# Performance work log

Hardware: AMD Instinct MI355X
Metric: run time of the kernel (lower is better)

Reference implementation:

```python
import jax, jax.numpy as jnp
import numpy as np

N = 100000   # nodes
E = 3200000  # edges (avg degree 32)
G = 1024     # graphs in batch
H = 16       # hidden_dim


def setup_inputs() -> dict:
    key = jax.random.key(0)
    ks = jax.random.split(key, 12)
    p = lambda k, s: jax.random.normal(k, s, dtype=jnp.float32) * 0.1
    return {
        "types": jax.random.randint(ks[0], (N,), 0, 3),
        "pos": jax.random.randint(ks[1], (N,), 0, 3),
        "edge_index": jax.random.randint(ks[2], (2, E), 0, N),
        "batch": jnp.sort(jax.random.randint(ks[3], (N,), 0, G)),
        "W1": p(ks[4], (3, H)), "b1": jnp.zeros((H,), jnp.float32),
        "W2": p(ks[5], (3, H)), "b2": jnp.zeros((H,), jnp.float32),
        "Wg0": p(ks[6], (2 * H, H)), "bg0": jnp.zeros((H,), jnp.float32),
        "Wg1": p(ks[7], (H, H)), "bg1": jnp.zeros((H,), jnp.float32),
        "Wg2": p(ks[8], (H, H)), "bg2": jnp.zeros((H,), jnp.float32),
        "Wo": p(ks[9], (H, 1)), "bo": jnp.zeros((1,), jnp.float32),
    }


def reference(types, pos, edge_index, batch, W1, b1, W2, b2,
              Wg0, bg0, Wg1, bg1, Wg2, bg2, Wo, bo):
    # one-hot encode + linear embed
    xt = jax.nn.one_hot(types, 3, dtype=jnp.float32) @ W1 + b1   # [N, H]
    xp = jax.nn.one_hot(pos, 3, dtype=jnp.float32) @ W2 + b2     # [N, H]
    z = jnp.concatenate([xt, xp], axis=-1)                        # [N, 2H]

    src, dst = edge_index[0], edge_index[1]
    # GCN symmetric normalization with self-loops (gcn_norm)
    deg = jax.ops.segment_sum(jnp.ones((E,), jnp.float32), dst, num_segments=N) + 1.0
    dis = jax.lax.rsqrt(deg)                                      # D^{-1/2}
    edge_coef = (dis[src] * dis[dst])[:, None]                    # [E, 1]
    self_coef = (dis * dis)[:, None]                              # [N, 1]

    def gcn_conv(x, W, b):
        h = x @ W                                                 # [N, H]
        agg = jax.ops.segment_sum(h[src] * edge_coef, dst, num_segments=N)
        return agg + h * self_coef + b

    z = jax.nn.relu(gcn_conv(z, Wg0, bg0))  # dropout=0.2 is train-only; eval mode
    z = jax.nn.relu(gcn_conv(z, Wg1, bg1))
    z = gcn_conv(z, Wg2, bg2)               # no act after last layer

    # global_mean_pool over graph ids
    cnt = jax.ops.segment_sum(jnp.ones((N,), jnp.float32), batch, num_segments=G)
    pooled = jax.ops.segment_sum(z, batch, num_segments=G) / jnp.maximum(cnt, 1.0)[:, None]
    return pooled @ Wo + bo                                       # [G, 1]
```

## Files before the change

kernel.cpp:

```cpp
#include <hip/hip_runtime.h>
#include <hip/hip_fp16.h>

#define NN 100000
#define NE 3200000
#define NG 1024
#define NP 100352
#define NBUCK 391
#define NBLK 256
#define CHUNK ((NE + NBLK - 1) / NBLK)
#define WINCAP 12288

static __device__ inline void acc_u2(float4& acc, uint2 u) {
    __half2* ph = reinterpret_cast<__half2*>(&u);
    float2 lo = __half22float2(ph[0]);
    float2 hi = __half22float2(ph[1]);
    acc.x += lo.x; acc.y += lo.y; acc.z += hi.x; acc.w += hi.y;
}
static __device__ inline uint2 pack4(float a, float b, float c, float d) {
    __half2 lo = __floats2half2_rn(a, b);
    __half2 hi = __floats2half2_rn(c, d);
    uint2 u;
    u.x = *reinterpret_cast<unsigned int*>(&lo);
    u.y = *reinterpret_cast<unsigned int*>(&hi);
    return u;
}
static __device__ inline float4 shfl_xor4(float4 v, int m) {
    float4 r;
    r.x = __shfl_xor(v.x, m); r.y = __shfl_xor(v.y, m);
    r.z = __shfl_xor(v.z, m); r.w = __shfl_xor(v.w, m);
    return r;
}

__global__ void hist_buckets(const int* __restrict__ dst, int* __restrict__ bcnt) {
    __shared__ int sm[NBUCK];
    int tid = threadIdx.x;
    for (int i = tid; i < NBUCK; i += 256) sm[i] = 0;
    __syncthreads();
    int s = blockIdx.x * CHUNK, e = min(NE, s + CHUNK);
    for (int i = s + tid; i < e; i += 256) atomicAdd(&sm[dst[i] >> 8], 1);
    __syncthreads();
    for (int i = tid; i < NBUCK; i += 256)
        if (sm[i]) atomicAdd(&bcnt[i], sm[i]);
}

__global__ void scan_buckets(const int* __restrict__ bcnt, int* __restrict__ bbase) {
    __shared__ int tmp[512];
    int tid = threadIdx.x;
    int v = (tid < NBUCK) ? bcnt[tid] : 0;
    tmp[tid] = v;
    __syncthreads();
    for (int off = 1; off < 512; off <<= 1) {
        int t = (tid >= off) ? tmp[tid - off] : 0;
        __syncthreads();
        tmp[tid] += t;
        __syncthreads();
    }
    if (tid < NBUCK) bbase[tid] = tmp[tid] - v;
}

__global__ void partition(const int* __restrict__ src, const int* __restrict__ dst,
                          const int* __restrict__ bbase, int* __restrict__ bfill,
                          int* __restrict__ part) {
    __shared__ int smh[NBUCK];
    __shared__ int smc[NBUCK];
    int tid = threadIdx.x;
    for (int i = tid; i < NBUCK; i += 256) smh[i] = 0;
    __syncthreads();
    int s = blockIdx.x * CHUNK, e = min(NE, s + CHUNK);
    for (int i = s + tid; i < e; i += 256) atomicAdd(&smh[dst[i] >> 8], 1);
    __syncthreads();
    for (int i = tid; i < NBUCK; i += 256) {
        int c = smh[i];
        smc[i] = c ? (bbase[i] + atomicAdd(&bfill[i], c)) : 0;
    }
    __syncthreads();
    for (int i = s + tid; i < e; i += 256) {
        int d = dst[i];
        int b = d >> 8;
        int p = atomicAdd(&smc[b], 1);
        part[p] = src[i] | ((d & 255) << 17);
    }
}

__global__ void build_csr(const int* __restrict__ part, const int* __restrict__ bbase,
                          const int* __restrict__ bcnt, int* __restrict__ cnt,
                          int* __restrict__ offs, float* __restrict__ dis,
                          int* __restrict__ srcs) {
    __shared__ int sm_cnt[256];
    __shared__ int sm_off[256];
    __shared__ int sm_cur[256];
    __shared__ int sm_win[WINCAP];
    int b = blockIdx.x, tid = threadIdx.x;
    int base = bbase[b], m = bcnt[b];
    sm_cnt[tid] = 0;
    __syncthreads();
    for (int i = tid; i < m; i += 256) atomicAdd(&sm_cnt[part[base + i] >> 17], 1);
    __syncthreads();
    int v = sm_cnt[tid];
    sm_off[tid] = v;
    __syncthreads();
    for (int off = 1; off < 256; off <<= 1) {
        int t = (tid >= off) ? sm_off[tid - off] : 0;
        __syncthreads();
        sm_off[tid] += t;
        __syncthreads();
    }
    int excl = sm_off[tid] - v;
    int n = b * 256 + tid;
    if (n < NN) {
        cnt[n] = v;
        offs[n] = base + excl;
        dis[n] = rsqrtf((float)v + 1.0f);
    }
    sm_cur[tid] = excl;
    __syncthreads();
    if (m <= WINCAP) {
        for (int i = tid; i < m; i += 256) {
            int p = part[base + i];
            int l = atomicAdd(&sm_cur[p >> 17], 1);
            sm_win[l] = p & 0x1FFFF;
        }
        __syncthreads();
        for (int i = tid; i < m; i += 256) srcs[base + i] = sm_win[i];
    } else {
        for (int i = tid; i < m; i += 256) {
            int p = part[base + i];
            int l = atomicAdd(&sm_cur[p >> 17], 1);
            srcs[base + l] = p & 0x1FFFF;
        }
    }
}

__global__ void embed_tf0(const int* __restrict__ types, const int* __restrict__ pos,
                          const float* __restrict__ W1, const float* __restrict__ b1,
                          const float* __restrict__ W2, const float* __restrict__ b2,
                          const float* __restrict__ Wg0, const float* __restrict__ dis,
                          uint2* __restrict__ hs) {
    __shared__ float sW[32 * 16];
    int tid = threadIdx.x;
    sW[tid] = Wg0[tid];
    sW[tid + 256] = Wg0[tid + 256];
    __syncthreads();
    int n = blockIdx.x * 256 + tid;
    if (n >= NN) return;
    int ty = types[n], pp = pos[n];
    float z[32];
#pragma unroll
    for (int j = 0; j < 16; j++) z[j] = W1[ty * 16 + j] + b1[j];
#pragma unroll
    for (int j = 0; j < 16; j++) z[16 + j] = W2[pp * 16 + j] + b2[j];
    float dn = dis[n];
    uint2 o[4];
#pragma unroll
    for (int q = 0; q < 4; q++) {
        float hv[4];
#pragma unroll
        for (int m = 0; m < 4; m++) {
            float a = 0.0f;
#pragma unroll
            for (int k = 0; k < 32; k++) a += z[k] * sW[k * 16 + q * 4 + m];
            hv[m] = a * dn;
        }
        o[q] = pack4(hv[0], hv[1], hv[2], hv[3]);
    }
#pragma unroll
    for (int q = 0; q < 4; q++) hs[(size_t)n * 4 + q] = o[q];
}

template <int RELU, int FUSE_POOL>
__global__ void agg_tf(const uint2* __restrict__ hs, const int* __restrict__ srcs,
                       const int* __restrict__ offs, const int* __restrict__ cnt,
                       const float* __restrict__ dis, const float* __restrict__ bias,
                       const float* __restrict__ Wn, uint2* __restrict__ hs_out,
                       const int* __restrict__ batch,
                       float* __restrict__ pool, int* __restrict__ gcnt) {
    __shared__ float sW[256];
    int tid = threadIdx.x;
    if (!FUSE_POOL) {
        sW[tid] = Wn[tid];
        __syncthreads();
    }
    int gid = blockIdx.x * 256 + tid;
    int n = gid >> 2, q = gid & 3;
    if (n >= NN) return;
    int beg = offs[n], deg = cnt[n];
    float dn = dis[n];
    float4 acc = make_float4(0.f, 0.f, 0.f, 0.f);
    int i = 0;
    for (; i + 4 <= deg; i += 4) {
        int s0 = srcs[beg + i + 0];
        int s1 = srcs[beg + i + 1];
        int s2 = srcs[beg + i + 2];
        int s3 = srcs[beg + i + 3];
        uint2 a0 = hs[(size_t)s0 * 4 + q];
        uint2 a1 = hs[(size_t)s1 * 4 + q];
        uint2 a2 = hs[(size_t)s2 * 4 + q];
        uint2 a3 = hs[(size_t)s3 * 4 + q];
        acc_u2(acc, a0); acc_u2(acc, a1); acc_u2(acc, a2); acc_u2(acc, a3);
    }
    for (; i < deg; i++) {
        int s = srcs[beg + i];
        acc_u2(acc, hs[(size_t)s * 4 + q]);
    }
    acc_u2(acc, hs[(size_t)n * 4 + q]);
    float4 b4 = ((const float4*)bias)[q];
    acc.x = fmaf(acc.x, dn, b4.x);
    acc.y = fmaf(acc.y, dn, b4.y);
    acc.z = fmaf(acc.z, dn, b4.z);
    acc.w = fmaf(acc.w, dn, b4.w);
    if (RELU) {
        acc.x = fmaxf(acc.x, 0.f); acc.y = fmaxf(acc.y, 0.f);
        acc.z = fmaxf(acc.z, 0.f); acc.w = fmaxf(acc.w, 0.f);
    }
    if (FUSE_POOL) {
        float4 w4 = ((const float4*)Wn)[q];
        float s = acc.x * w4.x + acc.y * w4.y + acc.z * w4.z + acc.w * w4.w;
        s += __shfl_xor(s, 1);
        s += __shfl_xor(s, 2);
        if (q == 0) {
            int g = batch[n];
            atomicAdd(&pool[g], s);
            atomicAdd(&gcnt[g], 1);
        }
    } else {
        float4 vals[4];
        vals[0] = acc;
        vals[1] = shfl_xor4(acc, 1);
        vals[2] = shfl_xor4(acc, 2);
        vals[3] = shfl_xor4(acc, 3);
        const float4* sW4 = (const float4*)sW;
        float4 hv = make_float4(0.f, 0.f, 0.f, 0.f);
#pragma unroll
        for (int m = 0; m < 4; m++) {
            float4 v = vals[m];
            int rb = (q ^ m) << 2;
            float4 w;
            w = sW4[(rb + 0) * 4 + q];
            hv.x += v.x * w.x; hv.y += v.x * w.y; hv.z += v.x * w.z; hv.w += v.x * w.w;
            w = sW4[(rb + 1) * 4 + q];
            hv.x += v.y * w.x; hv.y += v.y * w.y; hv.z += v.y * w.z; hv.w += v.y * w.w;
            w = sW4[(rb + 2) * 4 + q];
            hv.x += v.z * w.x; hv.y += v.z * w.y; hv.z += v.z * w.z; hv.w += v.z * w.w;
            w = sW4[(rb + 3) * 4 + q];
            hv.x += v.w * w.x; hv.y += v.w * w.y; hv.z += v.w * w.z; hv.w += v.w * w.w;
        }
        hs_out[(size_t)n * 4 + q] = pack4(hv.x * dn, hv.y * dn, hv.z * dn, hv.w * dn);
    }
}

__global__ void finalize(const float* __restrict__ pool, const int* __restrict__ gcnt,
                         const float* __restrict__ bo, float* __restrict__ out) {
    int g = blockIdx.x * 256 + threadIdx.x;
    if (g < NG) {
        float c = fmaxf((float)gcnt[g], 1.0f);
        out[g] = pool[g] / c + bo[0];
    }
}

extern "C" void kernel_launch(void* const* d_in, const int* in_sizes, int n_in,
                              void* d_out, int out_size, void* d_ws, size_t ws_size,
                              hipStream_t stream) {
    const int*   types = (const int*)d_in[0];
    const int*   pos   = (const int*)d_in[1];
    const int*   ei    = (const int*)d_in[2];
    const int*   batch = (const int*)d_in[3];
    const float* W1  = (const float*)d_in[4];
    const float* b1  = (const float*)d_in[5];
    const float* W2  = (const float*)d_in[6];
    const float* b2  = (const float*)d_in[7];
    const float* Wg0 = (const float*)d_in[8];
    const float* bg0 = (const float*)d_in[9];
    const float* Wg1 = (const float*)d_in[10];
    const float* bg1 = (const float*)d_in[11];
    const float* Wg2 = (const float*)d_in[12];
    const float* bg2 = (const float*)d_in[13];
    const float* Wo  = (const float*)d_in[14];
    const float* bo  = (const float*)d_in[15];
    float* out = (float*)d_out;

    const int* esrc = ei;
    const int* edst = ei + NE;

    int*   bcnt  = (int*)d_ws;
    int*   bfill = bcnt + 512;
    float* pool  = (float*)(bfill + 512);
    int*   gcnt  = (int*)(pool + NG);
    int*   bbase = gcnt + NG;
    int*   cnt   = bbase + 512;
    int*   offs  = cnt + NP;
    float* dis   = (float*)(offs + NP);
    int*   srcs  = (int*)(dis + NP);
    int*   part  = srcs + NE;
    uint2* hsA   = (uint2*)part;
    uint2* hsB   = (uint2*)(part + NE / 2);
    (void)ws_size; (void)n_in; (void)in_sizes; (void)out_size;

    hipMemsetAsync(d_ws, 0, (size_t)(1024 + 2 * NG) * sizeof(int), stream);

    const int NB256 = (NN + 255) / 256;
    const int QB = (NN * 4 + 255) / 256;

    hist_buckets<<<NBLK, 256, 0, stream>>>(edst, bcnt);
    scan_buckets<<<1, 512, 0, stream>>>(bcnt, bbase);
    partition<<<NBLK, 256, 0, stream>>>(esrc, edst, bbase, bfill, part);
    build_csr<<<NBUCK, 256, 0, stream>>>(part, bbase, bcnt, cnt, offs, dis, srcs);

    embed_tf0<<<NB256, 256, 0, stream>>>(types, pos, W1, b1, W2, b2, Wg0, dis, hsA);
    agg_tf<1, 0><<<QB, 256, 0, stream>>>(hsA, srcs, offs, cnt, dis, bg0, Wg1, hsB,
                                         batch, pool, gcnt);
    agg_tf<1, 0><<<QB, 256, 0, stream>>>(hsB, srcs, offs, cnt, dis, bg1, Wg2, hsA,
                                         batch, pool, gcnt);
    agg_tf<0, 1><<<QB, 256, 0, stream>>>(hsA, srcs, offs, cnt, dis, bg2, Wo, hsB ,
                                         batch, pool, gcnt);

    finalize<<<(NG + 255) / 256, 256, 0, stream>>>(pool, gcnt, bo, out);
}
```

Measured before the change: 333.5 us.

## Replace CSR gather with bucketed edge-parallel LDS-atomic aggregation

Drops the per-node CSR build (scan and reorder into srcs) and aggregates directly from the bucket-partitioned edge list. Each block, split four ways per 256-node bucket, accumulates 16-wide rows into shared memory with atomics, then flushes to a global fp32 buffer with global atomics. A separate per-node kernel applies bias, ReLU and the next weight matrix. This removes the CSR construction pass and the per-node degree imbalance, at the cost of heavy LDS atomic traffic, extra global atomics, a 6.4MB fp32 intermediate that is read and rezeroed each layer, and more kernel launches.

```diff
diff --git a/kernel.cpp b/kernel.cpp
--- a/kernel.cpp
+++ b/kernel.cpp
@@ -8,14 +8,8 @@
 #define NBUCK 391
 #define NBLK 256
 #define CHUNK ((NE + NBLK - 1) / NBLK)
-#define WINCAP 12288
-
-static __device__ inline void acc_u2(float4& acc, uint2 u) {
-    __half2* ph = reinterpret_cast<__half2*>(&u);
-    float2 lo = __half22float2(ph[0]);
-    float2 hi = __half22float2(ph[1]);
-    acc.x += lo.x; acc.y += lo.y; acc.z += hi.x; acc.w += hi.y;
-}
+#define SPLIT_LOG2 2
+
 static __device__ inline uint2 pack4(float a, float b, float c, float d) {
     __half2 lo = __floats2half2_rn(a, b);
     __half2 hi = __floats2half2_rn(c, d);
@@ -24,12 +18,6 @@
     u.y = *reinterpret_cast<unsigned int*>(&hi);
     return u;
 }
-static __device__ inline float4 shfl_xor4(float4 v, int m) {
-    float4 r;
-    r.x = __shfl_xor(v.x, m); r.y = __shfl_xor(v.y, m);
-    r.z = __shfl_xor(v.z, m); r.w = __shfl_xor(v.w, m);
-    return r;
-}
 
 __global__ void hist_buckets(const int* __restrict__ dst, int* __restrict__ bcnt) {
     __shared__ int sm[NBUCK];
@@ -82,53 +70,17 @@
     }
 }
 
-__global__ void build_csr(const int* __restrict__ part, const int* __restrict__ bbase,
-                          const int* __restrict__ bcnt, int* __restrict__ cnt,
-                          int* __restrict__ offs, float* __restrict__ dis,
-                          int* __restrict__ srcs) {
-    __shared__ int sm_cnt[256];
-    __shared__ int sm_off[256];
-    __shared__ int sm_cur[256];
-    __shared__ int sm_win[WINCAP];
+__global__ void deg_dis(const int* __restrict__ part, const int* __restrict__ bbase,
+                        const int* __restrict__ bcnt, float* __restrict__ dis) {
+    __shared__ int smc[256];
     int b = blockIdx.x, tid = threadIdx.x;
+    smc[tid] = 0;
+    __syncthreads();
     int base = bbase[b], m = bcnt[b];
-    sm_cnt[tid] = 0;
-    __syncthreads();
-    for (int i = tid; i < m; i += 256) atomicAdd(&sm_cnt[part[base + i] >> 17], 1);
-    __syncthreads();
-    int v = sm_cnt[tid];
-    sm_off[tid] = v;
-    __syncthreads();
-    for (int off = 1; off < 256; off <<= 1) {
-        int t = (tid >= off) ? sm_off[tid - off] : 0;
-        __syncthreads();
-        sm_off[tid] += t;
-        __syncthreads();
-    }
-    int excl = sm_off[tid] - v;
+    for (int i = base + tid; i < base + m; i += 256) atomicAdd(&smc[part[i] >> 17], 1);
+    __syncthreads();
     int n = b * 256 + tid;
-    if (n < NN) {
-        cnt[n] = v;
-        offs[n] = base + excl;
-        dis[n] = rsqrtf((float)v + 1.0f);
-    }
-    sm_cur[tid] = excl;
-    __syncthreads();
-    if (m <= WINCAP) {
-        for (int i = tid; i < m; i += 256) {
-            int p = part[base + i];
-            int l = atomicAdd(&sm_cur[p >> 17], 1);
-            sm_win[l] = p & 0x1FFFF;
-        }
-        __syncthreads();
-        for (int i = tid; i < m; i += 256) srcs[base + i] = sm_win[i];
-    } else {
-        for (int i = tid; i < m; i += 256) {
-            int p = part[base + i];
-            int l = atomicAdd(&sm_cur[p >> 17], 1);
-            srcs[base + l] = p & 0x1FFFF;
-        }
-    }
+    if (n < NN) dis[n] = rsqrtf((float)smc[tid] + 1.0f);
 }
 
 __global__ void embed_tf0(const int* __restrict__ types, const int* __restrict__ pos,
@@ -167,84 +119,135 @@
     for (int q = 0; q < 4; q++) hs[(size_t)n * 4 + q] = o[q];
 }
 
+static __device__ inline void acc16(float* __restrict__ ap, uint4 a, uint4 b) {
+    const __half2* h = reinterpret_cast<const __half2*>(&a);
+    const __half2* g = reinterpret_cast<const __half2*>(&b);
+    float2 f0 = __half22float2(h[0]), f1 = __half22float2(h[1]);
+    float2 f2 = __half22float2(h[2]), f3 = __half22float2(h[3]);
+    float2 f4 = __half22float2(g[0]), f5 = __half22float2(g[1]);
+    float2 f6 = __half22float2(g[2]), f7 = __half22float2(g[3]);
+    atomicAdd(ap + 0, f0.x);  atomicAdd(ap + 1, f0.y);
+    atomicAdd(ap + 2, f1.x);  atomicAdd(ap + 3, f1.y);
+    atomicAdd(ap + 4, f2.x);  atomicAdd(ap + 5, f2.y);
+    atomicAdd(ap + 6, f3.x);  atomicAdd(ap + 7, f3.y);
+    atomicAdd(ap + 8, f4.x);  atomicAdd(ap + 9, f4.y);
+    atomicAdd(ap + 10, f5.x); atomicAdd(ap + 11, f5.y);
+    atomicAdd(ap + 12, f6.x); atomicAdd(ap + 13, f6.y);
+    atomicAdd(ap + 14, f7.x); atomicAdd(ap + 15, f7.y);
+}
+
+__global__ __launch_bounds__(256, 4) void agg_edge(
+        const uint2* __restrict__ hs, const int* __restrict__ part,
+        const int* __restrict__ bbase, const int* __restrict__ bcnt,
+        float* __restrict__ zagg) {
+    __shared__ float acc[256 * 17];
+    int tid = threadIdx.x;
+    int b = blockIdx.x >> SPLIT_LOG2;
+    int s = blockIdx.x & ((1 << SPLIT_LOG2) - 1);
+    for (int i = tid; i < 256 * 17; i += 256) acc[i] = 0.f;
+    __syncthreads();
+    int base = bbase[b], m = bcnt[b];
+    int s0 = (int)(((long long)m * s) >> SPLIT_LOG2);
+    int s1 = (int)(((long long)m * (s + 1)) >> SPLIT_LOG2);
+    int i = base + s0 + tid;
+    int end = base + s1;
+
+    for (; i + 768 < end; i += 1024) {
+        int p0 = part[i];
+        int p1 = part[i + 256];
+        int p2 = part[i + 512];
+        int p3 = part[i + 768];
+        const uint4* q0 = (const uint4*)(hs + (size_t)(p0 & 0x1FFFF) * 4);
+        const uint4* q1 = (const uint4*)(hs + (size_t)(p1 & 0x1FFFF) * 4);
+        const uint4* q2 = (const uint4*)(hs + (size_t)(p2 & 0x1FFFF) * 4);
+        const uint4* q3 = (const uint4*)(hs + (size_t)(p3 & 0x1FFFF) * 4);
+        uint4 a0 = q0[0], b0 = q0[1];
+        uint4 a1 = q1[0], b1 = q1[1];
+        uint4 a2 = q2[0], b2 = q2[1];
+        uint4 a3 = q3[0], b3 = q3[1];
+        acc16(acc + (p0 >> 17) * 17, a0, b0);
+        acc16(acc + (p1 >> 17) * 17, a1, b1);
+        acc16(acc + (p2 >> 17) * 17, a2, b2);
+        acc16(acc + (p3 >> 17) * 17, a3, b3);
+    }
+    for (; i < end; i += 256) {
+        int p = part[i];
+        const uint4* q = (const uint4*)(hs + (size_t)(p & 0x1FFFF) * 4);
+        uint4 a = q[0], bb = q[1];
+        acc16(acc + (p >> 17) * 17, a, bb);
+    }
+    __syncthreads();
+
+    float* zb = zagg + (size_t)b * 4096;
+    for (int f = tid; f < 4096; f += 256) {
+        float v = acc[(f >> 4) * 17 + (f & 15)];
+        atomicAdd(zb + f, v);
+    }
+}
+
 template <int RELU, int FUSE_POOL>
-__global__ void agg_tf(const uint2* __restrict__ hs, const int* __restrict__ srcs,
-                       const int* __restrict__ offs, const int* __restrict__ cnt,
-                       const float* __restrict__ dis, const float* __restrict__ bias,
-                       const float* __restrict__ Wn, uint2* __restrict__ hs_out,
-                       const int* __restrict__ batch,
-                       float* __restrict__ pool, int* __restrict__ gcnt) {
+__global__ void tf_node(float* __restrict__ zagg, const uint2* __restrict__ hs,
+                        const float* __restrict__ dis, const float* __restrict__ bias,
+                        const float* __restrict__ Wn, uint2* __restrict__ hs_out,
+                        const int* __restrict__ batch, float* __restrict__ pool,
+                        int* __restrict__ gcnt) {
     __shared__ float sW[256];
     int tid = threadIdx.x;
     if (!FUSE_POOL) {
         sW[tid] = Wn[tid];
         __syncthreads();
     }
-    int gid = blockIdx.x * 256 + tid;
-    int n = gid >> 2, q = gid & 3;
+    int n = blockIdx.x * 256 + tid;
     if (n >= NN) return;
-    int beg = offs[n], deg = cnt[n];
+    float4* zp = (float4*)(zagg + (size_t)n * 16);
+    float4 z0 = zp[0], z1 = zp[1], z2 = zp[2], z3 = zp[3];
+    const uint4* hp = (const uint4*)(hs + (size_t)n * 4);
+    uint4 ha = hp[0], hb = hp[1];
+    if (!FUSE_POOL) {
+        float4 zero4 = make_float4(0.f, 0.f, 0.f, 0.f);
+        zp[0] = zero4; zp[1] = zero4; zp[2] = zero4; zp[3] = zero4;
+    }
     float dn = dis[n];
-    float4 acc = make_float4(0.f, 0.f, 0.f, 0.f);
-    int i = 0;
-    for (; i + 4 <= deg; i += 4) {
-        int s0 = srcs[beg + i + 0];
-        int s1 = srcs[beg + i + 1];
-        int s2 = srcs[beg + i + 2];
-        int s3 = srcs[beg + i + 3];
-        uint2 a0 = hs[(size_t)s0 * 4 + q];
-        uint2 a1 = hs[(size_t)s1 * 4 + q];
-        uint2 a2 = hs[(size_t)s2 * 4 + q];
-        uint2 a3 = hs[(size_t)s3 * 4 + q];
-        acc_u2(acc, a0); acc_u2(acc, a1); acc_u2(acc, a2); acc_u2(acc, a3);
-    }
-    for (; i < deg; i++) {
-        int s = srcs[beg + i];
-        acc_u2(acc, hs[(size_t)s * 4 + q]);
-    }
-    acc_u2(acc, hs[(size_t)n * 4 + q]);
-    float4 b4 = ((const float4*)bias)[q];
-    acc.x = fmaf(acc.x, dn, b4.x);
-    acc.y = fmaf(acc.y, dn, b4.y);
-    acc.z = fmaf(acc.z, dn, b4.z);
-    acc.w = fmaf(acc.w, dn, b4.w);
-    if (RELU) {
-        acc.x = fmaxf(acc.x, 0.f); acc.y = fmaxf(acc.y, 0.f);
-        acc.z = fmaxf(acc.z, 0.f); acc.w = fmaxf(acc.w, 0.f);
+    const __half2* h = reinterpret_cast<const __half2*>(&ha);
+    const __half2* g = reinterpret_cast<const __half2*>(&hb);
+    float2 s0 = __half22float2(h[0]), s1 = __half22float2(h[1]);
+    float2 s2 = __half22float2(h[2]), s3 = __half22float2(h[3]);
+    float2 s4 = __half22float2(g[0]), s5 = __half22float2(g[1]);
+    float2 s6 = __half22float2(g[2]), s7 = __half22float2(g[3]);
+    float z[16];
+    z[0] = z0.x + s0.x;  z[1] = z0.y + s0.y;  z[2] = z0.z + s1.x;  z[3] = z0.w + s1.y;
+    z[4] = z1.x + s2.x;  z[5] = z1.y + s2.y;  z[6] = z1.z + s3.x;  z[7] = z1.w + s3.y;
+    z[8] = z2.x + s4.x;  z[9] = z2.y + s4.y;  z[10] = z2.z + s5.x; z[11] = z2.w + s5.y;
+    z[12] = z3.x + s6.x; z[13] = z3.y + s6.y; z[14] = z3.z + s7.x; z[15] = z3.w + s7.y;
+#pragma unroll
+    for (int j = 0; j < 16; j++) {
+        z[j] = fmaf(z[j], dn, bias[j]);
+        if (RELU) z[j] = fmaxf(z[j], 0.f);
     }
     if (FUSE_POOL) {
-        float4 w4 = ((const float4*)Wn)[q];
-        float s = acc.x * w4.x + acc.y * w4.y + acc.z * w4.z + acc.w * w4.w;
-        s += __shfl_xor(s, 1);
-        s += __shfl_xor(s, 2);
-        if (q == 0) {
-            int g = batch[n];
-            atomicAdd(&pool[g], s);
-            atomicAdd(&gcnt[g], 1);
+        float sacc = 0.f;
+#pragma unroll
+        for (int j = 0; j < 16; j++) sacc += z[j] * Wn[j];
+        int gg = batch[n];
+        atomicAdd(&pool[gg], sacc);
+        atomicAdd(&gcnt[gg], 1);
+    } else {
+        uint2 o[4];
+#pragma unroll
+        for (int q = 0; q < 4; q++) {
+            float hv[4];
+#pragma unroll
+            for (int mm = 0; mm < 4; mm++) {
+                float a = 0.f;
+#pragma unroll
+                for (int k = 0; k < 16; k++) a += z[k] * sW[k * 16 + q * 4 + mm];
+                hv[mm] = a * dn;
+            }
+            o[q] = pack4(hv[0], hv[1], hv[2], hv[3]);
         }
-    } else {
-        float4 vals[4];
-        vals[0] = acc;
-        vals[1] = shfl_xor4(acc, 1);
-        vals[2] = shfl_xor4(acc, 2);
-        vals[3] = shfl_xor4(acc, 3);
-        const float4* sW4 = (const float4*)sW;
-        float4 hv = make_float4(0.f, 0.f, 0.f, 0.f);
-#pragma unroll
-        for (int m = 0; m < 4; m++) {
-            float4 v = vals[m];
-            int rb = (q ^ m) << 2;
-            float4 w;
-            w = sW4[(rb + 0) * 4 + q];
-            hv.x += v.x * w.x; hv.y += v.x * w.y; hv.z += v.x * w.z; hv.w += v.x * w.w;
-            w = sW4[(rb + 1) * 4 + q];
-            hv.x += v.y * w.x; hv.y += v.y * w.y; hv.z += v.y * w.z; hv.w += v.y * w.w;
-            w = sW4[(rb + 2) * 4 + q];
-            hv.x += v.z * w.x; hv.y += v.z * w.y; hv.z += v.z * w.z; hv.w += v.z * w.w;
-            w = sW4[(rb + 3) * 4 + q];
-            hv.x += v.w * w.x; hv.y += v.w * w.y; hv.z += v.w * w.z; hv.w += v.w * w.w;
-        }
-        hs_out[(size_t)n * 4 + q] = pack4(hv.x * dn, hv.y * dn, hv.z * dn, hv.w * dn);
+        uint2* op = hs_out + (size_t)n * 4;
+#pragma unroll
+        for (int q = 0; q < 4; q++) op[q] = o[q];
     }
 }
 
@@ -286,32 +289,34 @@
     float* pool  = (float*)(bfill + 512);
     int*   gcnt  = (int*)(pool + NG);
     int*   bbase = gcnt + NG;
-    int*   cnt   = bbase + 512;
-    int*   offs  = cnt + NP;
-    float* dis   = (float*)(offs + NP);
-    int*   srcs  = (int*)(dis + NP);
-    int*   part  = srcs + NE;
-    uint2* hsA   = (uint2*)part;
-    uint2* hsB   = (uint2*)(part + NE / 2);
+    float* dis   = (float*)(bbase + 512);
+    int*   part  = (int*)(dis + NP);
+    float* zagg  = (float*)(part + NE);
+    uint2* hsA   = (uint2*)(zagg + (size_t)NP * 16);
+    uint2* hsB   = (uint2*)((int*)hsA + NP * 8);
     (void)ws_size; (void)n_in; (void)in_sizes; (void)out_size;
 
     hipMemsetAsync(d_ws, 0, (size_t)(1024 + 2 * NG) * sizeof(int), stream);
+    hipMemsetAsync(zagg, 0, (size_t)NP * 16 * sizeof(float), stream);
 
     const int NB256 = (NN + 255) / 256;
-    const int QB = (NN * 4 + 255) / 256;
 
     hist_buckets<<<NBLK, 256, 0, stream>>>(edst, bcnt);
     scan_buckets<<<1, 512, 0, stream>>>(bcnt, bbase);
     partition<<<NBLK, 256, 0, stream>>>(esrc, edst, bbase, bfill, part);
-    build_csr<<<NBUCK, 256, 0, stream>>>(part, bbase, bcnt, cnt, offs, dis, srcs);
+    deg_dis<<<NBUCK, 256, 0, stream>>>(part, bbase, bcnt, dis);
 
     embed_tf0<<<NB256, 256, 0, stream>>>(types, pos, W1, b1, W2, b2, Wg0, dis, hsA);
-    agg_tf<1, 0><<<QB, 256, 0, stream>>>(hsA, srcs, offs, cnt, dis, bg0, Wg1, hsB,
-                                         batch, pool, gcnt);
-    agg_tf<1, 0><<<QB, 256, 0, stream>>>(hsB, srcs, offs, cnt, dis, bg1, Wg2, hsA,
-                                         batch, pool, gcnt);
-    agg_tf<0, 1><<<QB, 256, 0, stream>>>(hsA, srcs, offs, cnt, dis, bg2, Wo, hsB ,
-                                         batch, pool, gcnt);
+
+    agg_edge<<<NBUCK << SPLIT_LOG2, 256, 0, stream>>>(hsA, part, bbase, bcnt, zagg);
+    tf_node<1, 0><<<NB256, 256, 0, stream>>>(zagg, hsA, dis, bg0, Wg1, hsB,
+                                             batch, pool, gcnt);
+    agg_edge<<<NBUCK << SPLIT_LOG2, 256, 0, stream>>>(hsB, part, bbase, bcnt, zagg);
+    tf_node<1, 0><<<NB256, 256, 0, stream>>>(zagg, hsB, dis, bg1, Wg2, hsA,
+                                             batch, pool, gcnt);
+    agg_edge<<<NBUCK << SPLIT_LOG2, 256, 0, stream>>>(hsA, part, bbase, bcnt, zagg);
+    tf_node<0, 1><<<NB256, 256, 0, stream>>>(zagg, hsA, dis, bg2, Wo, hsB ,
+                                             batch, pool, gcnt);
 
     finalize<<<(NG + 255) / 256, 256, 0, stream>>>(pool, gcnt, bo, out);
 }
```

Result: slower. 1.154 ms (+246.0%).

## Split each node's edge list across two thread groups with vectorized index loads

Applied to the files above, without the earlier changes.

The aggregation kernel now assigns 8 threads per node instead of 4, splitting the edge range into two halves that are reduced with a cross-lane shuffle. Source indices are read as aligned 16-byte nontemporal vector loads with a one-step prefetch, after scalar handling of the misaligned head and leftover tail. The aim is more memory-level parallelism and fewer index load instructions in the gather-bound layers. In exchange the kernel launches twice as many threads, adds shuffle and branch overhead, and gives the two halves uneven work on low-degree nodes.

```diff
diff --git a/kernel.cpp b/kernel.cpp
--- a/kernel.cpp
+++ b/kernel.cpp
@@ -9,6 +9,8 @@
 #define NBLK 256
 #define CHUNK ((NE + NBLK - 1) / NBLK)
 #define WINCAP 12288
+
+typedef int v4i __attribute__((ext_vector_type(4)));
 
 static __device__ inline void acc_u2(float4& acc, uint2 u) {
     __half2* ph = reinterpret_cast<__half2*>(&u);
@@ -181,28 +183,52 @@
         __syncthreads();
     }
     int gid = blockIdx.x * 256 + tid;
-    int n = gid >> 2, q = gid & 3;
+    int n = gid >> 3, t = gid & 7;
+    int q = t & 3, h = t >> 2;
     if (n >= NN) return;
     int beg = offs[n], deg = cnt[n];
     float dn = dis[n];
+    const uint2* __restrict__ hq = hs + q;
     float4 acc = make_float4(0.f, 0.f, 0.f, 0.f);
-    int i = 0;
-    for (; i + 4 <= deg; i += 4) {
-        int s0 = srcs[beg + i + 0];
-        int s1 = srcs[beg + i + 1];
-        int s2 = srcs[beg + i + 2];
-        int s3 = srcs[beg + i + 3];
-        uint2 a0 = hs[(size_t)s0 * 4 + q];
-        uint2 a1 = hs[(size_t)s1 * 4 + q];
-        uint2 a2 = hs[(size_t)s2 * 4 + q];
-        uint2 a3 = hs[(size_t)s3 * 4 + q];
-        acc_u2(acc, a0); acc_u2(acc, a1); acc_u2(acc, a2); acc_u2(acc, a3);
-    }
-    for (; i < deg; i++) {
-        int s = srcs[beg + i];
-        acc_u2(acc, hs[(size_t)s * 4 + q]);
-    }
-    acc_u2(acc, hs[(size_t)n * 4 + q]);
+
+    int mis = (4 - (beg & 3)) & 3;
+    int pre = min(mis, deg);
+    if (h == 0) {
+        for (int i = 0; i < pre; i++) {
+            int s = srcs[beg + i];
+            acc_u2(acc, hq[(size_t)s * 4]);
+        }
+    }
+    int rem = deg - pre;
+    int nch = rem >> 2;
+    int abase = beg + pre;
+    const v4i* sp = (const v4i*)(srcs + abase);
+    int nch0 = nch >> 1;
+    int c0 = h ? nch0 : 0;
+    int c1 = h ? nch : nch0;
+    if (c0 < c1) {
+        v4i s = __builtin_nontemporal_load(sp + c0);
+        for (int c = c0; c < c1; c++) {
+            v4i sN = __builtin_nontemporal_load(sp + min(c + 1, c1 - 1));
+            uint2 g0 = hq[(size_t)s.x * 4];
+            uint2 g1 = hq[(size_t)s.y * 4];
+            uint2 g2 = hq[(size_t)s.z * 4];
+            uint2 g3 = hq[(size_t)s.w * 4];
+            acc_u2(acc, g0); acc_u2(acc, g1); acc_u2(acc, g2); acc_u2(acc, g3);
+            s = sN;
+        }
+    }
+    if (h == 1) {
+        for (int i = abase + nch * 4; i < beg + deg; i++) {
+            int s = srcs[i];
+            acc_u2(acc, hq[(size_t)s * 4]);
+        }
+    }
+
+    float4 o4 = shfl_xor4(acc, 4);
+    acc.x += o4.x; acc.y += o4.y; acc.z += o4.z; acc.w += o4.w;
+
+    acc_u2(acc, hq[(size_t)n * 4]);
     float4 b4 = ((const float4*)bias)[q];
     acc.x = fmaf(acc.x, dn, b4.x);
     acc.y = fmaf(acc.y, dn, b4.y);
@@ -217,7 +243,7 @@
         float s = acc.x * w4.x + acc.y * w4.y + acc.z * w4.z + acc.w * w4.w;
         s += __shfl_xor(s, 1);
         s += __shfl_xor(s, 2);
-        if (q == 0) {
+        if (t == 0) {
             int g = batch[n];
             atomicAdd(&pool[g], s);
             atomicAdd(&gcnt[g], 1);
@@ -244,7 +270,8 @@
             w = sW4[(rb + 3) * 4 + q];
             hv.x += v.w * w.x; hv.y += v.w * w.y; hv.z += v.w * w.z; hv.w += v.w * w.w;
         }
-        hs_out[(size_t)n * 4 + q] = pack4(hv.x * dn, hv.y * dn, hv.z * dn, hv.w * dn);
+        if (h == 0)
+            hs_out[(size_t)n * 4 + q] = pack4(hv.x * dn, hv.y * dn, hv.z * dn, hv.w * dn);
     }
 }
 
@@ -298,7 +325,7 @@
     hipMemsetAsync(d_ws, 0, (size_t)(1024 + 2 * NG) * sizeof(int), stream);
 
     const int NB256 = (NN + 255) / 256;
-    const int QB = (NN * 4 + 255) / 256;
+    const int QB8 = (NN * 8 + 255) / 256;
 
     hist_buckets<<<NBLK, 256, 0, stream>>>(edst, bcnt);
     scan_buckets<<<1, 512, 0, stream>>>(bcnt, bbase);
@@ -306,12 +333,12 @@
     build_csr<<<NBUCK, 256, 0, stream>>>(part, bbase, bcnt, cnt, offs, dis, srcs);
 
     embed_tf0<<<NB256, 256, 0, stream>>>(types, pos, W1, b1, W2, b2, Wg0, dis, hsA);
-    agg_tf<1, 0><<<QB, 256, 0, stream>>>(hsA, srcs, offs, cnt, dis, bg0, Wg1, hsB,
-                                         batch, pool, gcnt);
-    agg_tf<1, 0><<<QB, 256, 0, stream>>>(hsB, srcs, offs, cnt, dis, bg1, Wg2, hsA,
-                                         batch, pool, gcnt);
-    agg_tf<0, 1><<<QB, 256, 0, stream>>>(hsA, srcs, offs, cnt, dis, bg2, Wo, hsB ,
-                                         batch, pool, gcnt);
+    agg_tf<1, 0><<<QB8, 256, 0, stream>>>(hsA, srcs, offs, cnt, dis, bg0, Wg1, hsB,
+                                          batch, pool, gcnt);
+    agg_tf<1, 0><<<QB8, 256, 0, stream>>>(hsB, srcs, offs, cnt, dis, bg1, Wg2, hsA,
+                                          batch, pool, gcnt);
+    agg_tf<0, 1><<<QB8, 256, 0, stream>>>(hsA, srcs, offs, cnt, dis, bg2, Wo, hsB ,
+                                          batch, pool, gcnt);
 
     finalize<<<(NG + 255) / 256, 256, 0, stream>>>(pool, gcnt, bo, out);
 }
```

After: 352.0 us. +5.5%, slower.

## Aggregate first GCN layer over 9 input classes instead of dense features

Applied to the files above, without the earlier changes.

Each node's input embedding depends only on (type,pos), which has 9 combinations. The first layer therefore gathers a packed 4-byte word per neighbour (class id plus half-precision D^-1/2), accumulates 9 class-weighted sums, and applies a precomputed 9x16 table, replacing the 16-wide fp16 feature gather. Embedding and layer-0 aggregation are fused into one kernel that also applies Wg1, which removes the embed kernel and one hidden-state round trip. In exchange there are more ALU selects per edge, and dis is rounded to half precision for neighbour terms.

```diff
diff --git a/kernel.cpp b/kernel.cpp
--- a/kernel.cpp
+++ b/kernel.cpp
@@ -83,9 +83,10 @@
 }
 
 __global__ void build_csr(const int* __restrict__ part, const int* __restrict__ bbase,
-                          const int* __restrict__ bcnt, int* __restrict__ cnt,
+                          const int* __restrict__ bcnt, const int* __restrict__ types,
+                          const int* __restrict__ pos, int* __restrict__ cnt,
                           int* __restrict__ offs, float* __restrict__ dis,
-                          int* __restrict__ srcs) {
+                          unsigned int* __restrict__ pk, int* __restrict__ srcs) {
     __shared__ int sm_cnt[256];
     __shared__ int sm_off[256];
     __shared__ int sm_cur[256];
@@ -110,7 +111,11 @@
     if (n < NN) {
         cnt[n] = v;
         offs[n] = base + excl;
-        dis[n] = rsqrtf((float)v + 1.0f);
+        float dv = rsqrtf((float)v + 1.0f);
+        dis[n] = dv;
+        int cls = types[n] * 3 + pos[n];
+        __half hd = __float2half_rn(dv);
+        pk[n] = ((unsigned int)cls << 16) | (unsigned int)__half_as_ushort(hd);
     }
     sm_cur[tid] = excl;
     __syncthreads();
@@ -131,40 +136,96 @@
     }
 }
 
-__global__ void embed_tf0(const int* __restrict__ types, const int* __restrict__ pos,
-                          const float* __restrict__ W1, const float* __restrict__ b1,
-                          const float* __restrict__ W2, const float* __restrict__ b2,
-                          const float* __restrict__ Wg0, const float* __restrict__ dis,
-                          uint2* __restrict__ hs) {
-    __shared__ float sW[32 * 16];
-    int tid = threadIdx.x;
-    sW[tid] = Wg0[tid];
-    sW[tid + 256] = Wg0[tid + 256];
-    __syncthreads();
-    int n = blockIdx.x * 256 + tid;
+__global__ void agg0_tf(const unsigned int* __restrict__ pk,
+                        const int* __restrict__ srcs, const int* __restrict__ offs,
+                        const int* __restrict__ cnt, const float* __restrict__ dis,
+                        const float* __restrict__ W1, const float* __restrict__ b1,
+                        const float* __restrict__ W2, const float* __restrict__ b2,
+                        const float* __restrict__ Wg0, const float* __restrict__ bg0,
+                        const float* __restrict__ Wg1, uint2* __restrict__ hs_out) {
+    __shared__ float sV[144];
+    __shared__ float sW[256];
+    int tid = threadIdx.x;
+    sW[tid] = Wg1[tid];
+    if (tid < 144) {
+        int c = tid >> 4, f = tid & 15;
+        int ty = c / 3, pp = c % 3;
+        float a = 0.f;
+#pragma unroll
+        for (int k = 0; k < 16; k++) a += (W1[ty * 16 + k] + b1[k]) * Wg0[k * 16 + f];
+#pragma unroll
+        for (int k = 0; k < 16; k++) a += (W2[pp * 16 + k] + b2[k]) * Wg0[(16 + k) * 16 + f];
+        sV[tid] = a;
+    }
+    __syncthreads();
+    int gid = blockIdx.x * 256 + tid;
+    int n = gid >> 1, h = gid & 1;
     if (n >= NN) return;
-    int ty = types[n], pp = pos[n];
-    float z[32];
-#pragma unroll
-    for (int j = 0; j < 16; j++) z[j] = W1[ty * 16 + j] + b1[j];
-#pragma unroll
-    for (int j = 0; j < 16; j++) z[16 + j] = W2[pp * 16 + j] + b2[j];
+    int beg = offs[n], deg = cnt[n];
+    int half = deg >> 1;
+    int lo = beg + (h ? half : 0);
+    int hi = beg + (h ? deg : half);
+
+    float a0 = 0.f, a1 = 0.f, a2 = 0.f, a3 = 0.f, a4 = 0.f;
+    float a5 = 0.f, a6 = 0.f, a7 = 0.f, a8 = 0.f;
+#define ACCP(P)                                                       \
+    do {                                                              \
+        unsigned int _p = (P);                                        \
+        int _c = (int)(_p >> 16);                                     \
+        float _d = __half2float(__ushort_as_half((unsigned short)(_p & 0xFFFFu))); \
+        a0 += (_c == 0) ? _d : 0.f;  a1 += (_c == 1) ? _d : 0.f;      \
+        a2 += (_c == 2) ? _d : 0.f;  a3 += (_c == 3) ? _d : 0.f;      \
+        a4 += (_c == 4) ? _d : 0.f;  a5 += (_c == 5) ? _d : 0.f;      \
+        a6 += (_c == 6) ? _d : 0.f;  a7 += (_c == 7) ? _d : 0.f;      \
+        a8 += (_c == 8) ? _d : 0.f;                                   \
+    } while (0)
+    int i = lo;
+    for (; i + 4 <= hi; i += 4) {
+        int s0 = srcs[i + 0];
+        int s1 = srcs[i + 1];
+        int s2 = srcs[i + 2];
+        int s3 = srcs[i + 3];
+        unsigned int p0 = pk[s0];
+        unsigned int p1 = pk[s1];
+        unsigned int p2 = pk[s2];
+        unsigned int p3 = pk[s3];
+        ACCP(p0); ACCP(p1); ACCP(p2); ACCP(p3);
+    }
+    for (; i < hi; i++) ACCP(pk[srcs[i]]);
+
+    a0 += __shfl_xor(a0, 1); a1 += __shfl_xor(a1, 1); a2 += __shfl_xor(a2, 1);
+    a3 += __shfl_xor(a3, 1); a4 += __shfl_xor(a4, 1); a5 += __shfl_xor(a5, 1);
+    a6 += __shfl_xor(a6, 1); a7 += __shfl_xor(a7, 1); a8 += __shfl_xor(a8, 1);
+    ACCP(pk[n]);
+#undef ACCP
+
     float dn = dis[n];
-    uint2 o[4];
-#pragma unroll
-    for (int q = 0; q < 4; q++) {
-        float hv[4];
-#pragma unroll
-        for (int m = 0; m < 4; m++) {
-            float a = 0.0f;
-#pragma unroll
-            for (int k = 0; k < 32; k++) a += z[k] * sW[k * 16 + q * 4 + m];
-            hv[m] = a * dn;
-        }
-        o[q] = pack4(hv[0], hv[1], hv[2], hv[3]);
-    }
-#pragma unroll
-    for (int q = 0; q < 4; q++) hs[(size_t)n * 4 + q] = o[q];
+    float acc[9] = {a0, a1, a2, a3, a4, a5, a6, a7, a8};
+    float pre[16];
+#pragma unroll
+    for (int f = 0; f < 16; f++) {
+        float a = 0.f;
+#pragma unroll
+        for (int c = 0; c < 9; c++) a += acc[c] * sV[c * 16 + f];
+        a = fmaf(a, dn, bg0[f]);
+        pre[f] = fmaxf(a, 0.f);
+    }
+    if (h == 0) {
+        float hv[16];
+#pragma unroll
+        for (int f2 = 0; f2 < 16; f2++) hv[f2] = 0.f;
+#pragma unroll
+        for (int f = 0; f < 16; f++) {
+            float z = pre[f];
+#pragma unroll
+            for (int f2 = 0; f2 < 16; f2++) hv[f2] += z * sW[f * 16 + f2];
+        }
+        uint2* op = hs_out + (size_t)n * 4;
+#pragma unroll
+        for (int q = 0; q < 4; q++)
+            op[q] = pack4(hv[q * 4] * dn, hv[q * 4 + 1] * dn,
+                          hv[q * 4 + 2] * dn, hv[q * 4 + 3] * dn);
+    }
 }
 
 template <int RELU, int FUSE_POOL>
@@ -289,7 +350,8 @@
     int*   cnt   = bbase + 512;
     int*   offs  = cnt + NP;
     float* dis   = (float*)(offs + NP);
-    int*   srcs  = (int*)(dis + NP);
+    unsigned int* pk = (unsigned int*)(dis + NP);
+    int*   srcs  = (int*)(pk + NP);
     int*   part  = srcs + NE;
     uint2* hsA   = (uint2*)part;
     uint2* hsB   = (uint2*)(part + NE / 2);
@@ -297,21 +359,21 @@
 
     hipMemsetAsync(d_ws, 0, (size_t)(1024 + 2 * NG) * sizeof(int), stream);
 
-    const int NB256 = (NN + 255) / 256;
-    const int QB = (NN * 4 + 255) / 256;
+    const int QB  = (NN * 4 + 255) / 256;
+    const int QB2 = (NN * 2 + 255) / 256;
 
     hist_buckets<<<NBLK, 256, 0, stream>>>(edst, bcnt);
     scan_buckets<<<1, 512, 0, stream>>>(bcnt, bbase);
     partition<<<NBLK, 256, 0, stream>>>(esrc, edst, bbase, bfill, part);
-    build_csr<<<NBUCK, 256, 0, stream>>>(part, bbase, bcnt, cnt, offs, dis, srcs);
-
-    embed_tf0<<<NB256, 256, 0, stream>>>(types, pos, W1, b1, W2, b2, Wg0, dis, hsA);
-    agg_tf<1, 0><<<QB, 256, 0, stream>>>(hsA, srcs, offs, cnt, dis, bg0, Wg1, hsB,
+    build_csr<<<NBUCK, 256, 0, stream>>>(part, bbase, bcnt, types, pos,
+                                         cnt, offs, dis, pk, srcs);
+
+    agg0_tf<<<QB2, 256, 0, stream>>>(pk, srcs, offs, cnt, dis, W1, b1, W2, b2,
+                                     Wg0, bg0, Wg1, hsA);
+    agg_tf<1, 0><<<QB, 256, 0, stream>>>(hsA, srcs, offs, cnt, dis, bg1, Wg2, hsB,
                                          batch, pool, gcnt);
-    agg_tf<1, 0><<<QB, 256, 0, stream>>>(hsB, srcs, offs, cnt, dis, bg1, Wg2, hsA,
+    agg_tf<0, 1><<<QB, 256, 0, stream>>>(hsB, srcs, offs, cnt, dis, bg2, Wo, hsA ,
                                          batch, pool, gcnt);
-    agg_tf<0, 1><<<QB, 256, 0, stream>>>(hsA, srcs, offs, cnt, dis, bg2, Wo, hsB ,
-                                         batch, pool, gcnt);
 
     finalize<<<(NG + 255) / 256, 256, 0, stream>>>(pool, gcnt, bo, out);
 }
```

Result: faster. 325.7 us, median of 2 (-2.3%).
